# Kernel tuning notes

Measured on AMD Instinct MI355X. Metric: run time of the kernel, lower is better.

Reference implementation:

```python
import jax, jax.numpy as jnp
import numpy as np

B, LP, LQ, CL = 64, 64, 64, 8
VW, VC = 30002, 5002
WD, CD, CH, H, P = 300, 64, 64, 128, 20
EPS = 1e-6


def _norm(x, eps=EPS):
    # torch: sqrt(clamp(sum(x^2, -1), min=eps))
    return jnp.sqrt(jnp.maximum(jnp.sum(x * x, -1), eps))


def lstm_scan(x, Wih, Whh, b):
    # x: [N, T, D] -> outputs [N, T, Hh]; PyTorch gate order i,f,g,o
    N = x.shape[0]
    Hh = Whh.shape[1]
    xW = jnp.einsum('ntd,gd->ntg', x, Wih) + b  # precompute input projection
    def step(carry, xt):
        h, c = carry
        g = xt + h @ Whh.T
        i, f, gg, o = jnp.split(g, 4, axis=-1)
        c = jax.nn.sigmoid(f) * c + jax.nn.sigmoid(i) * jnp.tanh(gg)
        h = jax.nn.sigmoid(o) * jnp.tanh(c)
        return (h, c), h
    init = (jnp.zeros((N, Hh), x.dtype), jnp.zeros((N, Hh), x.dtype))
    _, hs = jax.lax.scan(step, init, jnp.swapaxes(xW, 0, 1))
    return jnp.swapaxes(hs, 0, 1)


def bilstm(x, Wf, Uf, bf, Wb, Ub, bb):
    fw = lstm_scan(x, Wf, Uf, bf)
    bw = jnp.flip(lstm_scan(jnp.flip(x, axis=1), Wb, Ub, bb), axis=1)
    return fw, bw


def mpm(p_fw, p_bw, q_fw, q_bw, ws):
    # ws: [8, P, H]
    def full(h1, h2, w):
        h1w = h1[:, :, None, :] * w              # [B,L,P,H]
        h2w = h2[:, -1, None, :] * w             # [B,P,H]
        num = jnp.einsum('blpd,bpd->blp', h1w, h2w)
        return num / _norm(h1w) / _norm(h2w)[:, None, :]
    def cos_matrix(x1, x2):
        num = jnp.einsum('bid,bjd->bij', x1, x2)
        return num / _norm(x1)[:, :, None] / _norm(x2)[:, None, :]
    def attentive(h1, h2, cm, w):
        h1w = h1[:, :, None, :] * w
        att = jnp.einsum('bij,bjd->bid', cm, h2) / (cm.sum(-1) + EPS)[..., None]
        attw = att[:, :, None, :] * w
        num = jnp.sum(h1w * attw, -1)
        return num / _norm(h1w) / _norm(attw)
    def max_attentive(h1, h2, cm, w):
        idx = jnp.argmax(cm, axis=-1)                           # [B,Lp]
        mv = jnp.take_along_axis(h2, idx[:, :, None], axis=1)   # [B,Lp,H]
        h1w = h1[:, :, None, :] * w
        mvw = mv[:, :, None, :] * w
        num = jnp.sum(h1w * mvw, -1)
        return num / _norm(h1w) / _norm(mvw)
    def max_pool(h1, h2, w):
        h1w = h1[:, :, None, :] * w
        h2w = h2[:, :, None, :] * w
        num = jnp.einsum('bipd,bjpd->bijp', h1w, h2w)           # [B,Lp,Lq,P]
        cos = num / _norm(h1w)[:, :, None, :] / _norm(h2w)[:, None, :, :]
        return cos.max(axis=2)
    cm_fw = cos_matrix(p_fw, q_fw)
    cm_bw = cos_matrix(p_bw, q_bw)
    return jnp.concatenate([
        full(p_fw, q_fw, ws[0]), full(p_bw, q_bw, ws[1]),
        attentive(p_fw, q_fw, cm_fw, ws[2]), attentive(p_bw, q_bw, cm_bw, ws[3]),
        max_attentive(p_fw, q_fw, cm_fw, ws[4]), max_attentive(p_bw, q_bw, cm_bw, ws[5]),
        max_pool(p_fw, q_fw, ws[6]), max_pool(p_bw, q_bw, ws[7])], axis=-1)


def setup_inputs():
    key = jax.random.key(0)
    ks = jax.random.split(key, 24)
    rn = lambda k, s, sc=0.1: jax.random.normal(k, s, dtype=jnp.float32) * sc
    def lstm_w(k, din, h):
        k1, k2 = jax.random.split(k)
        return rn(k1, (4 * h, din)), rn(k2, (4 * h, h)), jnp.zeros((4 * h,), jnp.float32)
    cWih, cWhh, cb = lstm_w(ks[4], CD, CH)
    xWf, xUf, xbf = lstm_w(ks[5], CH + WD, H)
    xWb, xUb, xbb = lstm_w(ks[6], CH + WD, H)
    aWf, aUf, abf = lstm_w(ks[7], 8 * P, H)
    aWb, aUb, abb = lstm_w(ks[8], 8 * P, H)
    return {
        'contentA_idxs': jax.random.randint(ks[0], (B, LP), 0, VW),
        'contentB_idxs': jax.random.randint(ks[1], (B, LQ), 0, VW),
        'contentA_char_idxs': jax.random.randint(ks[2], (B, LP, CL), 0, VC),
        'contentB_char_idxs': jax.random.randint(ks[3], (B, LQ, CL), 0, VC),
        'word_emb': rn(ks[9], (VW, WD), 1.0),
        'char_emb': rn(ks[10], (VC, CD), 1.0),
        'char_Wih': cWih, 'char_Whh': cWhh, 'char_b': cb,
        'ctx_Wih_f': xWf, 'ctx_Whh_f': xUf, 'ctx_b_f': xbf,
        'ctx_Wih_b': xWb, 'ctx_Whh_b': xUb, 'ctx_b_b': xbb,
        'agg_Wih_f': aWf, 'agg_Whh_f': aUf, 'agg_b_f': abf,
        'agg_Wih_b': aWb, 'agg_Whh_b': aUb, 'agg_b_b': abb,
        'mpm_w': rn(ks[11], (8, P, H), 1.0),
        'fc1_W': rn(ks[12], (2 * H, 4 * H), 0.005), 'fc1_b': jnp.zeros((2 * H,), jnp.float32),
        'fc2_W': rn(ks[13], (2, 2 * H), 0.005), 'fc2_b': jnp.zeros((2,), jnp.float32),
    }


def reference(contentA_idxs, contentB_idxs, contentA_char_idxs, contentB_char_idxs,
              word_emb, char_emb, char_Wih, char_Whh, char_b,
              ctx_Wih_f, ctx_Whh_f, ctx_b_f, ctx_Wih_b, ctx_Whh_b, ctx_b_b,
              agg_Wih_f, agg_Whh_f, agg_b_f, agg_Wih_b, agg_Whh_b, agg_b_b,
              mpm_w, fc1_W, fc1_b, fc2_W, fc2_b):
    def encode(word_idx, char_idx):
        w = word_emb[word_idx]                                   # [B,L,WD]
        L = word_idx.shape[1]
        c = char_emb[char_idx].reshape(B * L, CL, CD)
        ch = lstm_scan(c, char_Wih, char_Whh, char_b)[:, -1, :]  # last hidden
        x = jnp.concatenate([w, ch.reshape(B, L, CH)], axis=-1)
        return bilstm(x, ctx_Wih_f, ctx_Whh_f, ctx_b_f, ctx_Wih_b, ctx_Whh_b, ctx_b_b)
    p_fw, p_bw = encode(contentA_idxs, contentA_char_idxs)
    q_fw, q_bw = encode(contentB_idxs, contentB_char_idxs)
    mp = mpm(p_fw, p_bw, q_fw, q_bw, mpm_w)  # [B,LP,8P]
    mq = mpm(q_fw, q_bw, p_fw, p_bw, mpm_w)  # [B,LQ,8P]
    ap_fw, ap_bw = bilstm(mp, agg_Wih_f, agg_Whh_f, agg_b_f, agg_Wih_b, agg_Whh_b, agg_b_b)
    aq_fw, aq_bw = bilstm(mq, agg_Wih_f, agg_Whh_f, agg_b_f, agg_Wih_b, agg_Whh_b, agg_b_b)
    x = jnp.concatenate([ap_fw[:, -1], ap_bw[:, 0], aq_fw[:, -1], aq_bw[:, 0]], axis=-1)
    x = jnp.tanh(x @ fc1_W.T + fc1_b)
    return x @ fc2_W.T + fc2_b  # [B,2] logits
```

## Files before the change

### kernel.cpp

```cpp
#include <hip/hip_runtime.h>

#define EPS 1e-6f

typedef __attribute__((ext_vector_type(8))) short short8;
typedef __attribute__((ext_vector_type(8))) _Float16 half8;
typedef __attribute__((ext_vector_type(4))) float floatx4;

struct ScanArgs {
    const float* xw[4];
    const float* whh[4];
    float* out[4];
    int flipOut[4];
    int writeAll;
    int outStride;
};

struct MfArgs {
    const unsigned short* X;
    const unsigned short* W[4];
    const float* bias[4];
    float* out[4];
    int flip[4];
    int rowBase[4];
    int Kaug;
};

__device__ __forceinline__ float fsig(float x) { return 1.0f / (1.0f + __expf(-x)); }
__device__ __forceinline__ float tanh_fast(float x) {
    float e = __expf(2.f * x);
    return 1.f - 2.f / (e + 1.f);
}
__device__ __forceinline__ unsigned short f2bf(float x) {
    unsigned u = __float_as_uint(x);
    return (unsigned short)((u + 0x7fffu + ((u >> 16) & 1u)) >> 16);
}
__device__ __forceinline__ void split8_bf(const float* p, short8& hi, short8& lo) {
    #pragma unroll
    for (int e = 0; e < 8; ++e) {
        unsigned short h = f2bf(p[e]);
        float hf = __uint_as_float((unsigned)h << 16);
        hi[e] = (short)h;
        lo[e] = (short)f2bf(p[e] - hf);
    }
}
__device__ __forceinline__ void split8_f16(const float* p, half8& hi, half8& lo) {
    #pragma unroll
    for (int e = 0; e < 8; ++e) {
        _Float16 h = (_Float16)p[e];
        hi[e] = h;
        lo[e] = (_Float16)(p[e] - (float)h);
    }
}

__global__ void k_embed_word(const int* __restrict__ idxA, const int* __restrict__ idxB,
                             const float* __restrict__ emb,
                             float* __restrict__ xA, float* __restrict__ xB) {
    int row = blockIdx.x;
    const int* idx = (row < 4096) ? idxA : idxB;
    float* xout = (row < 4096) ? xA : xB;
    int r = row & 4095;
    size_t e = (size_t)idx[r];
    const float* src = emb + e * 300;
    float* dst = xout + (size_t)r * 364;
    for (int d = threadIdx.x; d < 300; d += blockDim.x) dst[d] = src[d];
}

__global__ void k_conv(const float* __restrict__ src, unsigned short* __restrict__ dst,
                       int K, int Ksec, int isW) {
    int row = blockIdx.x;
    const float* s = src + (size_t)row * K;
    unsigned short* d = dst + (size_t)row * (3 * Ksec);
    int o1 = (isW ? 2 : 1) * Ksec;
    int o2 = (isW ? 1 : 2) * Ksec;
    for (int k = threadIdx.x; k < Ksec; k += blockDim.x) {
        float x = (k < K) ? s[k] : 0.f;
        unsigned short hr = f2bf(x);
        float hif = __uint_as_float((unsigned)hr << 16);
        unsigned short lr2 = f2bf(x - hif);
        d[k]      = hr;
        d[o1 + k] = lr2;
        d[o2 + k] = hr;
    }
}

__global__ __launch_bounds__(256, 1)
void k_char_mfma(const int* __restrict__ cidxA, const int* __restrict__ cidxB,
                 const float* __restrict__ emb,
                 const unsigned short* __restrict__ WihA, const unsigned short* __restrict__ WhhA,
                 const float* __restrict__ bias,
                 float* __restrict__ xA, float* __restrict__ xB) {
    __shared__ __align__(16) float xs[32][68];
    __shared__ __align__(16) float hs[32][68];
    int tid = threadIdx.x;
    int w = tid >> 6, l = tid & 63, lr = l & 15, lc = l >> 4;
    int j = w * 16 + lr;
    short8 wih[4][6], whh[4][6];
    #pragma unroll
    for (int g = 0; g < 4; ++g)
        #pragma unroll
        for (int kt = 0; kt < 6; ++kt) {
            wih[g][kt] = *(const short8*)&WihA[(size_t)(g*64 + j)*192 + kt*32 + lc*8];
            whh[g][kt] = *(const short8*)&WhhA[(size_t)(g*64 + j)*192 + kt*32 + lc*8];
        }
    float bg[4];
    #pragma unroll
    for (int g = 0; g < 4; ++g) bg[g] = bias[g*64 + j];
    int seq0 = blockIdx.x * 32;
    for (int m = tid; m < 32*68; m += 256) (&hs[0][0])[m] = 0.f;
    float cst[2][4] = {};
    float hlast[2][4];
    __syncthreads();
    for (int t = 0; t < 8; ++t) {
        {
            int s = tid >> 3, ch = tid & 7;
            int sq = seq0 + s;
            const int* ci = (sq < 4096) ? cidxA : cidxB;
            int e = ci[(sq & 4095)*8 + t];
            float4 v0 = *(const float4*)&emb[(size_t)e*64 + ch*8];
            float4 v1 = *(const float4*)&emb[(size_t)e*64 + ch*8 + 4];
            *(float4*)&xs[s][ch*8] = v0;
            *(float4*)&xs[s][ch*8 + 4] = v1;
        }
        short8 hhi[2][2], hlo[2][2];
        if (t > 0) {
            #pragma unroll
            for (int mt = 0; mt < 2; ++mt)
                #pragma unroll
                for (int kt = 0; kt < 2; ++kt) {
                    float tmp[8];
                    *(float4*)&tmp[0] = *(const float4*)&hs[mt*16 + lr][kt*32 + lc*8];
                    *(float4*)&tmp[4] = *(const float4*)&hs[mt*16 + lr][kt*32 + lc*8 + 4];
                    split8_bf(tmp, hhi[mt][kt], hlo[mt][kt]);
                }
        }
        __syncthreads();
        short8 xhi[2][2], xlo[2][2];
        #pragma unroll
        for (int mt = 0; mt < 2; ++mt)
            #pragma unroll
            for (int kt = 0; kt < 2; ++kt) {
                float tmp[8];
                *(float4*)&tmp[0] = *(const float4*)&xs[mt*16 + lr][kt*32 + lc*8];
                *(float4*)&tmp[4] = *(const float4*)&xs[mt*16 + lr][kt*32 + lc*8 + 4];
                split8_bf(tmp, xhi[mt][kt], xlo[mt][kt]);
            }
        #pragma unroll
        for (int mt = 0; mt < 2; ++mt)
            #pragma unroll
            for (int g = 0; g < 4; ++g) {
                floatx4 a = {bg[g], bg[g], bg[g], bg[g]};
                a = __builtin_amdgcn_mfma_f32_16x16x32_bf16(xhi[mt][0], wih[g][0], a, 0, 0, 0);
                a = __builtin_amdgcn_mfma_f32_16x16x32_bf16(xhi[mt][1], wih[g][1], a, 0, 0, 0);
                a = __builtin_amdgcn_mfma_f32_16x16x32_bf16(xlo[mt][0], wih[g][2], a, 0, 0, 0);
                a = __builtin_amdgcn_mfma_f32_16x16x32_bf16(xlo[mt][1], wih[g][3], a, 0, 0, 0);
                a = __builtin_amdgcn_mfma_f32_16x16x32_bf16(xhi[mt][0], wih[g][4], a, 0, 0, 0);
                a = __builtin_amdgcn_mfma_f32_16x16x32_bf16(xhi[mt][1], wih[g][5], a, 0, 0, 0);
                if (t > 0) {
                    a = __builtin_amdgcn_mfma_f32_16x16x32_bf16(hhi[mt][0], whh[g][0], a, 0, 0, 0);
                    a = __builtin_amdgcn_mfma_f32_16x16x32_bf16(hhi[mt][1], whh[g][1], a, 0, 0, 0);
                    a = __builtin_amdgcn_mfma_f32_16x16x32_bf16(hlo[mt][0], whh[g][2], a, 0, 0, 0);
                    a = __builtin_amdgcn_mfma_f32_16x16x32_bf16(hlo[mt][1], whh[g][3], a, 0, 0, 0);
                    a = __builtin_amdgcn_mfma_f32_16x16x32_bf16(hhi[mt][0], whh[g][4], a, 0, 0, 0);
                    a = __builtin_amdgcn_mfma_f32_16x16x32_bf16(hhi[mt][1], whh[g][5], a, 0, 0, 0);
                }
                if (g == 0) { hlast[mt][0] = a[0]; hlast[mt][1] = a[1]; hlast[mt][2] = a[2]; hlast[mt][3] = a[3]; }
                else if (g == 1) {
                    #pragma unroll
                    for (int i = 0; i < 4; ++i) cst[mt][i] = fsig(a[i]) * cst[mt][i];
                } else if (g == 2) {
                    #pragma unroll
                    for (int i = 0; i < 4; ++i) cst[mt][i] += fsig(hlast[mt][i]) * tanh_fast(a[i]);
                } else {
                    #pragma unroll
                    for (int i = 0; i < 4; ++i) {
                        float h = fsig(a[i]) * tanh_fast(cst[mt][i]);
                        hlast[mt][i] = h;
                        hs[mt*16 + lc*4 + i][j] = h;
                    }
                }
            }
        __syncthreads();
    }
    #pragma unroll
    for (int mt = 0; mt < 2; ++mt)
        #pragma unroll
        for (int i = 0; i < 4; ++i) {
            int s = mt*16 + lc*4 + i;
            int sq = seq0 + s;
            float* xout = (sq < 4096) ? xA : xB;
            xout[(size_t)(sq & 4095)*364 + 300 + j] = hlast[mt][i];
        }
}

__global__ __launch_bounds__(256, 2)
void k_xw_mfma(MfArgs a) {
    int scan = blockIdx.z;
    const unsigned short* X = a.X;
    const unsigned short* W = a.W[scan];
    const float* bias = a.bias[scan];
    float* out = a.out[scan];
    int flip = a.flip[scan];
    int rowBase = a.rowBase[scan];
    int Kaug = a.Kaug;
    int m0 = blockIdx.x * 128;
    int n0 = blockIdx.y * 128;
    __shared__ __align__(16) unsigned short As[128][40];
    __shared__ __align__(16) unsigned short Bs[128][40];
    int tid = threadIdx.x;
    int wv = tid >> 6, lane = tid & 63;
    int lr = lane & 15, lc = lane >> 4;

    floatx4 acc[2][8];
    #pragma unroll
    for (int f = 0; f < 2; ++f)
        #pragma unroll
        for (int g = 0; g < 8; ++g)
            acc[f][g] = (floatx4){0.f, 0.f, 0.f, 0.f};

    int r0 = m0 + (tid >> 2);
    int r1 = r0 + 64;
    int sr0 = rowBase + (flip ? ((r0 & ~63) | (63 - (r0 & 63))) : r0);
    int sr1 = rowBase + (flip ? ((r1 & ~63) | (63 - (r1 & 63))) : r1);
    size_t asrc0 = (size_t)sr0 * Kaug + (tid & 3) * 8;
    size_t asrc1 = (size_t)sr1 * Kaug + (tid & 3) * 8;
    size_t bsrc0 = (size_t)(n0 + (tid >> 2)) * Kaug + (tid & 3) * 8;
    size_t bsrc1 = (size_t)(n0 + (tid >> 2) + 64) * Kaug + (tid & 3) * 8;
    int swrow = tid >> 2, swcol = (tid & 3) * 8;

    for (int k0 = 0; k0 < Kaug; k0 += 32) {
        short8 a0 = *(const short8*)(X + asrc0 + k0);
        short8 a1 = *(const short8*)(X + asrc1 + k0);
        short8 b0 = *(const short8*)(W + bsrc0 + k0);
        short8 b1 = *(const short8*)(W + bsrc1 + k0);
        __syncthreads();
        *(short8*)&As[swrow][swcol]      = a0;
        *(short8*)&As[swrow + 64][swcol] = a1;
        *(short8*)&Bs[swrow][swcol]      = b0;
        *(short8*)&Bs[swrow + 64][swcol] = b1;
        __syncthreads();
        short8 af0 = *(const short8*)&As[wv*32 + lr][lc*8];
        short8 af1 = *(const short8*)&As[wv*32 + 16 + lr][lc*8];
        #pragma unroll
        for (int g = 0; g < 8; ++g) {
            short8 bf = *(const short8*)&Bs[g*16 + lr][lc*8];
            acc[0][g] = __builtin_amdgcn_mfma_f32_16x16x32_bf16(af0, bf, acc[0][g], 0, 0, 0);
            acc[1][g] = __builtin_amdgcn_mfma_f32_16x16x32_bf16(af1, bf, acc[1][g], 0, 0, 0);
        }
    }

    #pragma unroll
    for (int f = 0; f < 2; ++f) {
        int row = m0 + wv*32 + f*16 + lc*4;
        #pragma unroll
        for (int g = 0; g < 8; ++g) {
            int col = n0 + g*16 + lr;
            float bv = bias[col];
            #pragma unroll
            for (int i = 0; i < 4; ++i)
                out[(size_t)(row + i)*512 + col] = acc[f][g][i] + bv;
        }
    }
}

__global__ __launch_bounds__(1024, 1)
void k_lstm_scan(ScanArgs a) {
    int b = blockIdx.x;
    int scan = blockIdx.y;
    int tid = threadIdx.x;
    int p = tid >> 9;
    int g = tid & 511;
    __shared__ __align__(16) float h_lds[128];
    __shared__ float gpart[2][512];
    const float* W = a.whh[scan] + (size_t)g*128 + p*64;
    float w[64];
    #pragma unroll
    for (int k4 = 0; k4 < 16; ++k4) {
        float4 v = *(const float4*)&W[k4*4];
        w[k4*4+0]=v.x; w[k4*4+1]=v.y; w[k4*4+2]=v.z; w[k4*4+3]=v.w;
    }
    const float* xw = a.xw[scan] + (size_t)b*64*512;
    float* outp = a.out[scan];
    int flip = a.flipOut[scan];
    int wAll = a.writeAll;
    float c = 0.f;
    if (tid < 128) h_lds[tid] = 0.f;
    __syncthreads();
    const float* hbase = &h_lds[p*64];
    for (int t = 0; t < 64; ++t) {
        float a0 = (p == 0) ? xw[t*512 + g] : 0.f;
        float a1 = 0.f, a2 = 0.f, a3 = 0.f;
        #pragma unroll
        for (int k16 = 0; k16 < 4; ++k16) {
            float4 h0 = *(const float4*)&hbase[k16*16+0];
            float4 h1 = *(const float4*)&hbase[k16*16+4];
            float4 h2 = *(const float4*)&hbase[k16*16+8];
            float4 h3 = *(const float4*)&hbase[k16*16+12];
            a0 += w[k16*16+ 0]*h0.x + w[k16*16+ 1]*h0.y + w[k16*16+ 2]*h0.z + w[k16*16+ 3]*h0.w;
            a1 += w[k16*16+ 4]*h1.x + w[k16*16+ 5]*h1.y + w[k16*16+ 6]*h1.z + w[k16*16+ 7]*h1.w;
            a2 += w[k16*16+ 8]*h2.x + w[k16*16+ 9]*h2.y + w[k16*16+10]*h2.z + w[k16*16+11]*h2.w;
            a3 += w[k16*16+12]*h3.x + w[k16*16+13]*h3.y + w[k16*16+14]*h3.z + w[k16*16+15]*h3.w;
        }
        gpart[p][g] = (a0+a1)+(a2+a3);
        __syncthreads();
        if (tid < 128) {
            float gi = gpart[0][tid]       + gpart[1][tid];
            float gf = gpart[0][128 + tid] + gpart[1][128 + tid];
            float gg = gpart[0][256 + tid] + gpart[1][256 + tid];
            float go = gpart[0][384 + tid] + gpart[1][384 + tid];
            c = fsig(gf)*c + fsig(gi)*tanhf(gg);
            float h = fsig(go)*tanhf(c);
            h_lds[tid] = h;
            if (wAll) {
                int tout = flip ? (63 - t) : t;
                outp[((size_t)b*64 + tout)*128 + tid] = h;
            }
        }
        __syncthreads();
    }
    if (!wAll && tid < 128)
        outp[(size_t)b * a.outStride + tid] = h_lds[tid];
}

__global__ __launch_bounds__(256, 1)
void k_cos_matrix(const float* __restrict__ pfw, const float* __restrict__ pbw,
                  const float* __restrict__ qfw, const float* __restrict__ qbw,
                  float* __restrict__ cmf, float* __restrict__ cmb) {
    int b = blockIdx.x, dir = blockIdx.y;
    const float* h1 = (dir ? pbw : pfw) + (size_t)b*8192;
    const float* h2 = (dir ? qbw : qfw) + (size_t)b*8192;
    float* cm = (dir ? cmb : cmf) + (size_t)b*4096;
    __shared__ __align__(16) float A[64][132];
    __shared__ __align__(16) float Bt[64][132];
    __shared__ float n1[64], n2[64];
    int tid = threadIdx.x;
    for (int m = tid; m < 8192; m += 256) {
        int r = m >> 7, d = m & 127;
        A[r][d] = h1[m];
        Bt[r][d] = h2[m];
    }
    __syncthreads();
    if (tid < 128) {
        const float* row = (tid < 64) ? &A[tid][0] : &Bt[tid-64][0];
        float s = 0.f;
        #pragma unroll
        for (int k4 = 0; k4 < 32; ++k4) {
            float4 v = *(const float4*)&row[k4*4];
            s += v.x*v.x + v.y*v.y + v.z*v.z + v.w*v.w;
        }
        float nv = sqrtf(fmaxf(s, EPS));
        if (tid < 64) n1[tid] = nv; else n2[tid-64] = nv;
    }
    __syncthreads();
    int tx = tid & 15, ty = tid >> 4;
    float acc[4][4] = {};
    #pragma unroll
    for (int k4 = 0; k4 < 32; ++k4) {
        float4 av[4], bv[4];
        #pragma unroll
        for (int i = 0; i < 4; ++i) av[i] = *(const float4*)&A[ty + i*16][k4*4];
        #pragma unroll
        for (int j = 0; j < 4; ++j) bv[j] = *(const float4*)&Bt[tx + j*16][k4*4];
        #pragma unroll
        for (int i = 0; i < 4; ++i)
            #pragma unroll
            for (int j = 0; j < 4; ++j)
                acc[i][j] += av[i].x*bv[j].x + av[i].y*bv[j].y + av[i].z*bv[j].z + av[i].w*bv[j].w;
    }
    #pragma unroll
    for (int i = 0; i < 4; ++i) {
        int r = ty + i*16;
        #pragma unroll
        for (int j = 0; j < 4; ++j) {
            int c2 = tx + j*16;
            cm[r*64 + c2] = acc[i][j] / (n1[r]*n2[c2]);
        }
    }
}

__global__ __launch_bounds__(512, 2)
void k_full_att(const float* __restrict__ pfw, const float* __restrict__ pbw,
                const float* __restrict__ qfw, const float* __restrict__ qbw,
                const float* __restrict__ cmf, const float* __restrict__ cmb,
                const float* __restrict__ mpmw,
                float* __restrict__ mp, float* __restrict__ mq) {
    int b = blockIdx.x, dir = blockIdx.y, which = blockIdx.z;
    const float* pd = (dir ? pbw : pfw) + (size_t)b*8192;
    const float* qd = (dir ? qbw : qfw) + (size_t)b*8192;
    const float* h1g = which ? qd : pd;
    const float* h2g = which ? pd : qd;
    const float* cmsrc = (dir ? cmb : cmf) + (size_t)b*4096;
    float* outb = which ? mq : mp;
    __shared__ __align__(16) float h2s[64][132];
    __shared__ float cms[64][68];
    __shared__ __align__(16) float wl[3*20*128];
    int tid = threadIdx.x;
    for (int m = tid; m < 8192; m += 512) {
        int r = m >> 7, d = m & 127;
        h2s[r][d] = h2g[m];
    }
    for (int m = tid; m < 4096; m += 512) {
        int l = m >> 6, j = m & 63;
        cms[l][j] = which ? cmsrc[j*64 + l] : cmsrc[m];
    }
    for (int m = tid; m < 2560; m += 512) {
        wl[m]        = mpmw[(size_t)(0+dir)*2560 + m];
        wl[2560 + m] = mpmw[(size_t)(2+dir)*2560 + m];
        wl[5120 + m] = mpmw[(size_t)(4+dir)*2560 + m];
    }
    __syncthreads();
    int l = tid >> 3, r = tid & 7;
    int d0 = r * 16;
    float h1d[16];
    #pragma unroll
    for (int q4 = 0; q4 < 4; ++q4) {
        float4 v = *(const float4*)&h1g[l*128 + d0 + q4*4];
        h1d[q4*4+0]=v.x; h1d[q4*4+1]=v.y; h1d[q4*4+2]=v.z; h1d[q4*4+3]=v.w;
    }
    float rsum = 0.f, bv = -3.4e38f; int bj = 64;
    for (int jj = 0; jj < 8; ++jj) {
        int j = r*8 + jj;
        float cv = cms[l][j];
        rsum += cv;
        if (cv > bv) { bv = cv; bj = j; }
    }
    #pragma unroll
    for (int m = 1; m < 8; m <<= 1) rsum += __shfl_xor(rsum, m, 8);
    #pragma unroll
    for (int m = 1; m < 8; m <<= 1) {
        float ov = __shfl_xor(bv, m, 8);
        int oj = __shfl_xor(bj, m, 8);
        if (ov > bv || (ov == bv && oj < bj)) { bv = ov; bj = oj; }
    }
    float att[16];
    #pragma unroll
    for (int dd = 0; dd < 16; ++dd) att[dd] = 0.f;
    for (int j = 0; j < 64; ++j) {
        float cv = cms[l][j];
        #pragma unroll
        for (int q4 = 0; q4 < 4; ++q4) {
            float4 hv = *(const float4*)&h2s[j][d0 + q4*4];
            att[q4*4+0] += cv*hv.x; att[q4*4+1] += cv*hv.y;
            att[q4*4+2] += cv*hv.z; att[q4*4+3] += cv*hv.w;
        }
    }
    float rinv = 1.f / (rsum + EPS);
    #pragma unroll
    for (int dd = 0; dd < 16; ++dd) att[dd] *= rinv;
    float mvd[16], h2l[16];
    #pragma unroll
    for (int q4 = 0; q4 < 4; ++q4) {
        float4 v = *(const float4*)&h2s[bj][d0 + q4*4];
        mvd[q4*4+0]=v.x; mvd[q4*4+1]=v.y; mvd[q4*4+2]=v.z; mvd[q4*4+3]=v.w;
        float4 u = *(const float4*)&h2s[63][d0 + q4*4];
        h2l[q4*4+0]=u.x; h2l[q4*4+1]=u.y; h2l[q4*4+2]=u.z; h2l[q4*4+3]=u.w;
    }
    size_t outrow = ((size_t)b*64 + l)*160;
    for (int pp = 0; pp < 20; ++pp) {
        const float* wf = &wl[pp*128 + d0];
        const float* wa = &wl[2560 + pp*128 + d0];
        const float* wm = &wl[5120 + pp*128 + d0];
        float fn=0,f1=0,f2=0, an=0,a1=0,a2=0, mn=0,m1=0,m2=0;
        #pragma unroll
        for (int dd = 0; dd < 16; ++dd) {
            float wfv = wf[dd], wav = wa[dd], wmv = wm[dd];
            float x1 = h1d[dd]*wfv, x2 = h2l[dd]*wfv;
            fn += x1*x2; f1 += x1*x1; f2 += x2*x2;
            float y1 = h1d[dd]*wav, y2 = att[dd]*wav;
            an += y1*y2; a1 += y1*y1; a2 += y2*y2;
            float z1 = h1d[dd]*wmv, z2 = mvd[dd]*wmv;
            mn += z1*z2; m1 += z1*z1; m2 += z2*z2;
        }
        #pragma unroll
        for (int m = 1; m < 8; m <<= 1) {
            fn += __shfl_xor(fn,m,8); f1 += __shfl_xor(f1,m,8); f2 += __shfl_xor(f2,m,8);
            an += __shfl_xor(an,m,8); a1 += __shfl_xor(a1,m,8); a2 += __shfl_xor(a2,m,8);
            mn += __shfl_xor(mn,m,8); m1 += __shfl_xor(m1,m,8); m2 += __shfl_xor(m2,m,8);
        }
        if (r == 0) {
            outb[outrow + (0+dir)*20 + pp] = fn / sqrtf(fmaxf(f1,EPS)) / sqrtf(fmaxf(f2,EPS));
            outb[outrow + (2+dir)*20 + pp] = an / sqrtf(fmaxf(a1,EPS)) / sqrtf(fmaxf(a2,EPS));
            outb[outrow + (4+dir)*20 + pp] = mn / sqrtf(fmaxf(m1,EPS)) / sqrtf(fmaxf(m2,EPS));
        }
    }
}

__global__ __launch_bounds__(256, 1)
void k_maxpool_mfma(const float* __restrict__ pfw, const float* __restrict__ pbw,
                    const float* __restrict__ qfw, const float* __restrict__ qbw,
                    const float* __restrict__ mpmw,
                    float* __restrict__ mp, float* __restrict__ mq) {
    int b = blockIdx.x, dir = blockIdx.y, pph = blockIdx.z;
    const float* h1 = (dir ? pbw : pfw) + (size_t)b*8192;
    const float* h2 = (dir ? qbw : qfw) + (size_t)b*8192;
    __shared__ __align__(16) float h1s[64][132];
    __shared__ __align__(16) float h2s[64][132];
    __shared__ __align__(16) float w2s[32][132];
    __shared__ float n1s[64][25], n2s[64][25];
    __shared__ float cpart[4][68];
    int tid = threadIdx.x;
    int w = tid >> 6, l = tid & 63, lr = l & 15, lc = l >> 4;
    for (int m = tid; m < 8192; m += 256) {
        int r = m >> 7, d = m & 127;
        h1s[r][d] = h1[m];
        h2s[r][d] = h2[m];
    }
    for (int m = tid; m < 32*128; m += 256) {
        int r = m >> 7, d = m & 127;
        float v = (r < 20) ? mpmw[(size_t)((6+dir)*20 + r)*128 + d] : 0.f;
        w2s[r][d] = v * v;
    }
    __syncthreads();
    float a1[32], b1[32];
    #pragma unroll
    for (int kt = 0; kt < 4; ++kt) {
        *(float4*)&a1[kt*8]     = *(const float4*)&h1s[w*16 + lr][kt*32 + lc*8];
        *(float4*)&a1[kt*8 + 4] = *(const float4*)&h1s[w*16 + lr][kt*32 + lc*8 + 4];
        *(float4*)&b1[kt*8]     = *(const float4*)&h2s[w*16 + lr][kt*32 + lc*8];
        *(float4*)&b1[kt*8 + 4] = *(const float4*)&h2s[w*16 + lr][kt*32 + lc*8 + 4];
    }
    half8 Bh[4][4], Bl[4][4];
    #pragma unroll
    for (int nt = 0; nt < 4; ++nt)
        #pragma unroll
        for (int kt = 0; kt < 4; ++kt) {
            float tmp[8];
            *(float4*)&tmp[0] = *(const float4*)&h2s[nt*16 + lr][kt*32 + lc*8];
            *(float4*)&tmp[4] = *(const float4*)&h2s[nt*16 + lr][kt*32 + lc*8 + 4];
            split8_f16(tmp, Bh[nt][kt], Bl[nt][kt]);
        }
    {
        float sq[32];
        half8 s1h[4], s1l[4], s2h[4], s2l[4];
        #pragma unroll
        for (int kt = 0; kt < 4; ++kt) {
            #pragma unroll
            for (int e = 0; e < 8; ++e) sq[kt*8+e] = a1[kt*8+e]*a1[kt*8+e];
            split8_f16(&sq[kt*8], s1h[kt], s1l[kt]);
        }
        #pragma unroll
        for (int kt = 0; kt < 4; ++kt) {
            #pragma unroll
            for (int e = 0; e < 8; ++e) sq[kt*8+e] = b1[kt*8+e]*b1[kt*8+e];
            split8_f16(&sq[kt*8], s2h[kt], s2l[kt]);
        }
        half8 w2h[2][4], w2l[2][4];
        #pragma unroll
        for (int nt2 = 0; nt2 < 2; ++nt2)
            #pragma unroll
            for (int kt = 0; kt < 4; ++kt) {
                float tmp[8];
                *(float4*)&tmp[0] = *(const float4*)&w2s[nt2*16 + lr][kt*32 + lc*8];
                *(float4*)&tmp[4] = *(const float4*)&w2s[nt2*16 + lr][kt*32 + lc*8 + 4];
                split8_f16(tmp, w2h[nt2][kt], w2l[nt2][kt]);
            }
        #pragma unroll
        for (int nt2 = 0; nt2 < 2; ++nt2) {
            floatx4 na1 = {0.f,0.f,0.f,0.f}, na2 = {0.f,0.f,0.f,0.f};
            #pragma unroll
            for (int kt = 0; kt < 4; ++kt) {
                na1 = __builtin_amdgcn_mfma_f32_16x16x32_f16(s1h[kt], w2h[nt2][kt], na1, 0, 0, 0);
                na2 = __builtin_amdgcn_mfma_f32_16x16x32_f16(s2h[kt], w2h[nt2][kt], na2, 0, 0, 0);
            }
            #pragma unroll
            for (int kt = 0; kt < 4; ++kt) {
                na1 = __builtin_amdgcn_mfma_f32_16x16x32_f16(s1l[kt], w2h[nt2][kt], na1, 0, 0, 0);
                na2 = __builtin_amdgcn_mfma_f32_16x16x32_f16(s2l[kt], w2h[nt2][kt], na2, 0, 0, 0);
            }
            #pragma unroll
            for (int kt = 0; kt < 4; ++kt) {
                na1 = __builtin_amdgcn_mfma_f32_16x16x32_f16(s1h[kt], w2l[nt2][kt], na1, 0, 0, 0);
                na2 = __builtin_amdgcn_mfma_f32_16x16x32_f16(s2h[kt], w2l[nt2][kt], na2, 0, 0, 0);
            }
            #pragma unroll
            for (int i = 0; i < 4; ++i) {
                int row = w*16 + lc*4 + i;
                int c2 = nt2*16 + lr;
                if (c2 < 20) {
                    n1s[row][c2] = sqrtf(fmaxf(na1[i], EPS));
                    n2s[row][c2] = sqrtf(fmaxf(na2[i], EPS));
                }
            }
        }
    }
    __syncthreads();
    for (int pi = 0; pi < 10; ++pi) {
        int pp = pph*10 + pi;
        int col = (6+dir)*20 + pp;
        half8 ah[4], al[4];
        #pragma unroll
        for (int kt = 0; kt < 4; ++kt) {
            float wv[8], aw[8];
            *(float4*)&wv[0] = *(const float4*)&w2s[pp][kt*32 + lc*8];
            *(float4*)&wv[4] = *(const float4*)&w2s[pp][kt*32 + lc*8 + 4];
            #pragma unroll
            for (int e = 0; e < 8; ++e) aw[e] = a1[kt*8+e]*wv[e];
            split8_f16(aw, ah[kt], al[kt]);
        }
        float n1v[4];
        #pragma unroll
        for (int i = 0; i < 4; ++i) n1v[i] = n1s[w*16 + lc*4 + i][pp];
        float rmax[4] = {-3.4e38f, -3.4e38f, -3.4e38f, -3.4e38f};
        float cmx[4];
        #pragma unroll
        for (int nt = 0; nt < 4; ++nt) {
            floatx4 acc = {0.f,0.f,0.f,0.f};
            #pragma unroll
            for (int kt = 0; kt < 4; ++kt)
                acc = __builtin_amdgcn_mfma_f32_16x16x32_f16(ah[kt], Bh[nt][kt], acc, 0, 0, 0);
            #pragma unroll
            for (int kt = 0; kt < 4; ++kt)
                acc = __builtin_amdgcn_mfma_f32_16x16x32_f16(al[kt], Bh[nt][kt], acc, 0, 0, 0);
            #pragma unroll
            for (int kt = 0; kt < 4; ++kt)
                acc = __builtin_amdgcn_mfma_f32_16x16x32_f16(ah[kt], Bl[nt][kt], acc, 0, 0, 0);
            float n2v = n2s[nt*16 + lr][pp];
            float cm_ = -3.4e38f;
            #pragma unroll
            for (int i = 0; i < 4; ++i) {
                float cv = acc[i] / (n1v[i] * n2v);
                rmax[i] = fmaxf(rmax[i], cv);
                cm_ = fmaxf(cm_, cv);
            }
            cmx[nt] = cm_;
        }
        #pragma unroll
        for (int msk = 1; msk < 16; msk <<= 1)
            #pragma unroll
            for (int i = 0; i < 4; ++i) rmax[i] = fmaxf(rmax[i], __shfl_xor(rmax[i], msk));
        if (lr == 0) {
            #pragma unroll
            for (int i = 0; i < 4; ++i)
                mp[((size_t)b*64 + w*16 + lc*4 + i)*160 + col] = rmax[i];
        }
        #pragma unroll
        for (int msk = 16; msk < 64; msk <<= 1)
            #pragma unroll
            for (int nt = 0; nt < 4; ++nt) cmx[nt] = fmaxf(cmx[nt], __shfl_xor(cmx[nt], msk));
        if (lc == 0) {
            #pragma unroll
            for (int nt = 0; nt < 4; ++nt) cpart[w][nt*16 + lr] = cmx[nt];
        }
        __syncthreads();
        if (tid < 64) {
            float mv = fmaxf(fmaxf(cpart[0][tid], cpart[1][tid]),
                             fmaxf(cpart[2][tid], cpart[3][tid]));
            mq[((size_t)b*64 + tid)*160 + col] = mv;
        }
        __syncthreads();
    }
}

__global__ void k_fc(const float* __restrict__ xcat,
                     const float* __restrict__ fc1W, const float* __restrict__ fc1b,
                     const float* __restrict__ fc2W, const float* __restrict__ fc2b,
                     float* __restrict__ out) {
    int b = blockIdx.x;
    int tid = threadIdx.x;
    __shared__ float y[256];
    const float* x = xcat + (size_t)b*512;
    float acc = fc1b[tid];
    #pragma unroll 8
    for (int k4 = 0; k4 < 128; ++k4) {
        float4 wv = *(const float4*)&fc1W[(size_t)tid*512 + k4*4];
        float4 xv = *(const float4*)&x[k4*4];
        acc += wv.x*xv.x + wv.y*xv.y + wv.z*xv.z + wv.w*xv.w;
    }
    y[tid] = tanhf(acc);
    __syncthreads();
    if (tid < 2) {
        float o = fc2b[tid];
        for (int k = 0; k < 256; ++k) o += y[k]*fc2W[tid*256 + k];
        out[b*2 + tid] = o;
    }
}

extern "C" void kernel_launch(void* const* d_in, const int* in_sizes, int n_in,
                              void* d_out, int out_size, void* d_ws, size_t ws_size,
                              hipStream_t stream) {
    (void)in_sizes; (void)n_in; (void)out_size; (void)ws_size;
    const int* idxA  = (const int*)d_in[0];
    const int* idxB  = (const int*)d_in[1];
    const int* cidxA = (const int*)d_in[2];
    const int* cidxB = (const int*)d_in[3];
    const float* wemb = (const float*)d_in[4];
    const float* cemb = (const float*)d_in[5];
    const float* cWih = (const float*)d_in[6];
    const float* cWhh = (const float*)d_in[7];
    const float* cb   = (const float*)d_in[8];
    const float* xWf = (const float*)d_in[9];
    const float* xUf = (const float*)d_in[10];
    const float* xbf = (const float*)d_in[11];
    const float* xWb = (const float*)d_in[12];
    const float* xUb = (const float*)d_in[13];
    const float* xbb = (const float*)d_in[14];
    const float* aWf = (const float*)d_in[15];
    const float* aUf = (const float*)d_in[16];
    const float* abf = (const float*)d_in[17];
    const float* aWb = (const float*)d_in[18];
    const float* aUb = (const float*)d_in[19];
    const float* abb = (const float*)d_in[20];
    const float* mpmw = (const float*)d_in[21];
    const float* fc1W = (const float*)d_in[22];
    const float* fc1b = (const float*)d_in[23];
    const float* fc2W = (const float*)d_in[24];
    const float* fc2b = (const float*)d_in[25];
    float* out = (float*)d_out;

    float* ws = (float*)d_ws;
    float* xA  = ws; ws += (size_t)4096*364;
    float* xB  = ws; ws += (size_t)4096*364;
    float* xw0 = ws; ws += (size_t)4096*512;
    float* xw1 = ws; ws += (size_t)4096*512;
    float* xw2 = ws; ws += (size_t)4096*512;
    float* xw3 = ws; ws += (size_t)4096*512;
    float* pfw = ws; ws += (size_t)4096*128;
    float* pbw = ws; ws += (size_t)4096*128;
    float* qfw = ws; ws += (size_t)4096*128;
    float* qbw = ws; ws += (size_t)4096*128;
    float* cmf = ws; ws += (size_t)64*64*64;
    float* cmb = ws; ws += (size_t)64*64*64;
    float* mp  = ws; ws += (size_t)4096*160;
    float* mq  = ws; ws += (size_t)4096*160;
    float* xcat = ws; ws += (size_t)64*512;
    unsigned short* Xaug = (unsigned short*)ws; ws += (size_t)8192*1152/2;
    unsigned short* Wfa  = (unsigned short*)ws; ws += (size_t)512*1152/2;
    unsigned short* Wba  = (unsigned short*)ws; ws += (size_t)512*1152/2;
    unsigned short* WihC = (unsigned short*)ws; ws += (size_t)256*192/2;
    unsigned short* WhhC = (unsigned short*)ws; ws += (size_t)256*192/2;

    k_conv<<<256, 128, 0, stream>>>(cWih, WihC, 64, 64, 1);
    k_conv<<<256, 128, 0, stream>>>(cWhh, WhhC, 64, 64, 1);
    k_embed_word<<<8192, 128, 0, stream>>>(idxA, idxB, wemb, xA, xB);
    k_char_mfma<<<256, 256, 0, stream>>>(cidxA, cidxB, cemb, WihC, WhhC, cb, xA, xB);
    k_conv<<<4096, 128, 0, stream>>>(xA, Xaug, 364, 384, 0);
    k_conv<<<4096, 128, 0, stream>>>(xB, Xaug + (size_t)4096*1152, 364, 384, 0);
    k_conv<<<512, 128, 0, stream>>>(xWf, Wfa, 364, 384, 1);
    k_conv<<<512, 128, 0, stream>>>(xWb, Wba, 364, 384, 1);
    MfArgs cx;
    cx.X = Xaug;
    cx.W[0]=Wfa; cx.W[1]=Wfa; cx.W[2]=Wba; cx.W[3]=Wba;
    cx.bias[0]=xbf; cx.bias[1]=xbf; cx.bias[2]=xbb; cx.bias[3]=xbb;
    cx.out[0]=xw0; cx.out[1]=xw1; cx.out[2]=xw2; cx.out[3]=xw3;
    cx.flip[0]=0; cx.flip[1]=0; cx.flip[2]=1; cx.flip[3]=1;
    cx.rowBase[0]=0; cx.rowBase[1]=4096; cx.rowBase[2]=0; cx.rowBase[3]=4096;
    cx.Kaug = 1152;
    k_xw_mfma<<<dim3(32, 4, 4), 256, 0, stream>>>(cx);
    ScanArgs cs;
    cs.xw[0]=xw0; cs.xw[1]=xw1; cs.xw[2]=xw2; cs.xw[3]=xw3;
    cs.whh[0]=xUf; cs.whh[1]=xUf; cs.whh[2]=xUb; cs.whh[3]=xUb;
    cs.out[0]=pfw; cs.out[1]=qfw; cs.out[2]=pbw; cs.out[3]=qbw;
    cs.flipOut[0]=0; cs.flipOut[1]=0; cs.flipOut[2]=1; cs.flipOut[3]=1;
    cs.writeAll = 1; cs.outStride = 0;
    k_lstm_scan<<<dim3(64, 4), 1024, 0, stream>>>(cs);
    k_cos_matrix<<<dim3(64, 2), 256, 0, stream>>>(pfw, pbw, qfw, qbw, cmf, cmb);
    k_full_att<<<dim3(64, 2, 2), 512, 0, stream>>>(pfw, pbw, qfw, qbw, cmf, cmb, mpmw, mp, mq);
    k_maxpool_mfma<<<dim3(64, 2, 2), 256, 0, stream>>>(pfw, pbw, qfw, qbw, mpmw, mp, mq);
    k_conv<<<4096, 128, 0, stream>>>(mp, Xaug, 160, 160, 0);
    k_conv<<<4096, 128, 0, stream>>>(mq, Xaug + (size_t)4096*480, 160, 160, 0);
    k_conv<<<512, 128, 0, stream>>>(aWf, Wfa, 160, 160, 1);
    k_conv<<<512, 128, 0, stream>>>(aWb, Wba, 160, 160, 1);
    MfArgs ax;
    ax.X = Xaug;
    ax.W[0]=Wfa; ax.W[1]=Wfa; ax.W[2]=Wba; ax.W[3]=Wba;
    ax.bias[0]=abf; ax.bias[1]=abf; ax.bias[2]=abb; ax.bias[3]=abb;
    ax.out[0]=xw0; ax.out[1]=xw1; ax.out[2]=xw2; ax.out[3]=xw3;
    ax.flip[0]=0; ax.flip[1]=0; ax.flip[2]=1; ax.flip[3]=1;
    ax.rowBase[0]=0; ax.rowBase[1]=4096; ax.rowBase[2]=0; ax.rowBase[3]=4096;
    ax.Kaug = 480;
    k_xw_mfma<<<dim3(32, 4, 4), 256, 0, stream>>>(ax);
    ScanArgs as;
    as.xw[0]=xw0; as.xw[1]=xw1; as.xw[2]=xw2; as.xw[3]=xw3;
    as.whh[0]=aUf; as.whh[1]=aUf; as.whh[2]=aUb; as.whh[3]=aUb;
    as.out[0]=xcat+0; as.out[1]=xcat+256; as.out[2]=xcat+128; as.out[3]=xcat+384;
    as.flipOut[0]=0; as.flipOut[1]=0; as.flipOut[2]=0; as.flipOut[3]=0;
    as.writeAll = 0; as.outStride = 512;
    k_lstm_scan<<<dim3(64, 4), 1024, 0, stream>>>(as);
    k_fc<<<64, 256, 0, stream>>>(xcat, fc1W, fc1b, fc2W, fc2b, out);
}
```

Measured before the change: 416.6 us.

## Fuse bf16 split conversion into embed/char kernels; packed FMA LSTM scan

The word-embedding gather and the char-LSTM epilogue now write the hi/lo/hi bf16-split augmented input directly, removing the fp32 xA/xB intermediates and two conversion launches. The LSTM scan kernel switches its recurrent dot product to v_pk_fma_f32 on float pairs and prefetches the next timestep's input projection. Its launch bounds change from 1 to 4 blocks per SM, which may limit registers and cause spills of the 64 weight values held per thread.

```diff
diff --git a/kernel.cpp b/kernel.cpp
--- a/kernel.cpp
+++ b/kernel.cpp
@@ -5,6 +5,7 @@
 typedef __attribute__((ext_vector_type(8))) short short8;
 typedef __attribute__((ext_vector_type(8))) _Float16 half8;
 typedef __attribute__((ext_vector_type(4))) float floatx4;
+typedef __attribute__((ext_vector_type(2))) float floatx2;
 
 struct ScanArgs {
     const float* xw[4];
@@ -51,18 +52,30 @@
         lo[e] = (_Float16)(p[e] - (float)h);
     }
 }
+__device__ __forceinline__ floatx2 pk_fma(floatx2 a, floatx2 b, floatx2 c) {
+    floatx2 d;
+    asm("v_pk_fma_f32 %0, %1, %2, %3" : "=v"(d) : "v"(a), "v"(b), "v"(c));
+    return d;
+}
 
 __global__ void k_embed_word(const int* __restrict__ idxA, const int* __restrict__ idxB,
                              const float* __restrict__ emb,
-                             float* __restrict__ xA, float* __restrict__ xB) {
+                             unsigned short* __restrict__ Xaug) {
     int row = blockIdx.x;
     const int* idx = (row < 4096) ? idxA : idxB;
-    float* xout = (row < 4096) ? xA : xB;
     int r = row & 4095;
     size_t e = (size_t)idx[r];
     const float* src = emb + e * 300;
-    float* dst = xout + (size_t)r * 364;
-    for (int d = threadIdx.x; d < 300; d += blockDim.x) dst[d] = src[d];
+    unsigned short* d = Xaug + (size_t)row * 1152;
+    for (int k = threadIdx.x; k < 384; k += blockDim.x) {
+        float x = (k < 300) ? src[k] : 0.f;
+        unsigned short hr = f2bf(x);
+        float hif = __uint_as_float((unsigned)hr << 16);
+        unsigned short lr2 = f2bf(x - hif);
+        d[k]       = hr;
+        d[384 + k] = lr2;
+        d[768 + k] = hr;
+    }
 }
 
 __global__ void k_conv(const float* __restrict__ src, unsigned short* __restrict__ dst,
@@ -88,7 +101,7 @@
                  const float* __restrict__ emb,
                  const unsigned short* __restrict__ WihA, const unsigned short* __restrict__ WhhA,
                  const float* __restrict__ bias,
-                 float* __restrict__ xA, float* __restrict__ xB) {
+                 unsigned short* __restrict__ Xaug) {
     __shared__ __align__(16) float xs[32][68];
     __shared__ __align__(16) float hs[32][68];
     int tid = threadIdx.x;
@@ -187,8 +200,15 @@
         for (int i = 0; i < 4; ++i) {
             int s = mt*16 + lc*4 + i;
             int sq = seq0 + s;
-            float* xout = (sq < 4096) ? xA : xB;
-            xout[(size_t)(sq & 4095)*364 + 300 + j] = hlast[mt][i];
+            unsigned short* d = Xaug + (size_t)sq * 1152;
+            float h = hlast[mt][i];
+            unsigned short hh = f2bf(h);
+            float hf = __uint_as_float((unsigned)hh << 16);
+            unsigned short hl = f2bf(h - hf);
+            int k = 300 + j;
+            d[k]       = hh;
+            d[384 + k] = hl;
+            d[768 + k] = hh;
         }
 }
 
@@ -262,7 +282,7 @@
     }
 }
 
-__global__ __launch_bounds__(1024, 1)
+__global__ __launch_bounds__(1024, 4)
 void k_lstm_scan(ScanArgs a) {
     int b = blockIdx.x;
     int scan = blockIdx.y;
@@ -272,12 +292,9 @@
     __shared__ __align__(16) float h_lds[128];
     __shared__ float gpart[2][512];
     const float* W = a.whh[scan] + (size_t)g*128 + p*64;
-    float w[64];
-    #pragma unroll
-    for (int k4 = 0; k4 < 16; ++k4) {
-        float4 v = *(const float4*)&W[k4*4];
-        w[k4*4+0]=v.x; w[k4*4+1]=v.y; w[k4*4+2]=v.z; w[k4*4+3]=v.w;
-    }
+    floatx2 w2[32];
+    #pragma unroll
+    for (int k = 0; k < 32; ++k) w2[k] = *(const floatx2*)&W[k*2];
     const float* xw = a.xw[scan] + (size_t)b*64*512;
     float* outp = a.out[scan];
     int flip = a.flipOut[scan];
@@ -285,22 +302,23 @@
     float c = 0.f;
     if (tid < 128) h_lds[tid] = 0.f;
     __syncthreads();
-    const float* hbase = &h_lds[p*64];
+    const float* hb = &h_lds[p*64];
+    float xwc = (p == 0) ? xw[g] : 0.f;
     for (int t = 0; t < 64; ++t) {
-        float a0 = (p == 0) ? xw[t*512 + g] : 0.f;
-        float a1 = 0.f, a2 = 0.f, a3 = 0.f;
-        #pragma unroll
-        for (int k16 = 0; k16 < 4; ++k16) {
-            float4 h0 = *(const float4*)&hbase[k16*16+0];
-            float4 h1 = *(const float4*)&hbase[k16*16+4];
-            float4 h2 = *(const float4*)&hbase[k16*16+8];
-            float4 h3 = *(const float4*)&hbase[k16*16+12];
-            a0 += w[k16*16+ 0]*h0.x + w[k16*16+ 1]*h0.y + w[k16*16+ 2]*h0.z + w[k16*16+ 3]*h0.w;
-            a1 += w[k16*16+ 4]*h1.x + w[k16*16+ 5]*h1.y + w[k16*16+ 6]*h1.z + w[k16*16+ 7]*h1.w;
-            a2 += w[k16*16+ 8]*h2.x + w[k16*16+ 9]*h2.y + w[k16*16+10]*h2.z + w[k16*16+11]*h2.w;
-            a3 += w[k16*16+12]*h3.x + w[k16*16+13]*h3.y + w[k16*16+14]*h3.z + w[k16*16+15]*h3.w;
-        }
-        gpart[p][g] = (a0+a1)+(a2+a3);
+        float xwn = 0.f;
+        if (p == 0 && t < 63) xwn = xw[(size_t)(t+1)*512 + g];
+        floatx2 a0 = {0.f,0.f}, a1 = {0.f,0.f}, a2 = {0.f,0.f}, a3 = {0.f,0.f};
+        #pragma unroll
+        for (int kk = 0; kk < 8; ++kk) {
+            floatx4 u = *(const floatx4*)&hb[kk*8];
+            floatx4 v = *(const floatx4*)&hb[kk*8 + 4];
+            a0 = pk_fma(w2[kk*4+0], __builtin_shufflevector(u, u, 0, 1), a0);
+            a1 = pk_fma(w2[kk*4+1], __builtin_shufflevector(u, u, 2, 3), a1);
+            a2 = pk_fma(w2[kk*4+2], __builtin_shufflevector(v, v, 0, 1), a2);
+            a3 = pk_fma(w2[kk*4+3], __builtin_shufflevector(v, v, 2, 3), a3);
+        }
+        float s = ((a0.x + a0.y) + (a1.x + a1.y)) + ((a2.x + a2.y) + (a3.x + a3.y));
+        gpart[p][g] = xwc + s;
         __syncthreads();
         if (tid < 128) {
             float gi = gpart[0][tid]       + gpart[1][tid];
@@ -316,6 +334,7 @@
             }
         }
         __syncthreads();
+        xwc = xwn;
     }
     if (!wAll && tid < 128)
         outp[(size_t)b * a.outStride + tid] = h_lds[tid];
@@ -707,8 +726,6 @@
     float* out = (float*)d_out;
 
     float* ws = (float*)d_ws;
-    float* xA  = ws; ws += (size_t)4096*364;
-    float* xB  = ws; ws += (size_t)4096*364;
     float* xw0 = ws; ws += (size_t)4096*512;
     float* xw1 = ws; ws += (size_t)4096*512;
     float* xw2 = ws; ws += (size_t)4096*512;
@@ -730,10 +747,8 @@
 
     k_conv<<<256, 128, 0, stream>>>(cWih, WihC, 64, 64, 1);
     k_conv<<<256, 128, 0, stream>>>(cWhh, WhhC, 64, 64, 1);
-    k_embed_word<<<8192, 128, 0, stream>>>(idxA, idxB, wemb, xA, xB);
-    k_char_mfma<<<256, 256, 0, stream>>>(cidxA, cidxB, cemb, WihC, WhhC, cb, xA, xB);
-    k_conv<<<4096, 128, 0, stream>>>(xA, Xaug, 364, 384, 0);
-    k_conv<<<4096, 128, 0, stream>>>(xB, Xaug + (size_t)4096*1152, 364, 384, 0);
+    k_embed_word<<<8192, 128, 0, stream>>>(idxA, idxB, wemb, Xaug);
+    k_char_mfma<<<256, 256, 0, stream>>>(cidxA, cidxB, cemb, WihC, WhhC, cb, Xaug);
     k_conv<<<512, 128, 0, stream>>>(xWf, Wfa, 364, 384, 1);
     k_conv<<<512, 128, 0, stream>>>(xWb, Wba, 364, 384, 1);
     MfArgs cx;
```

Result: faster. 368.6 us (median of 2 runs) (-11.5%).
